# Optimization experiments

Hardware: AMD Instinct MI355X
Metric: run time of the kernel (lower is better)

The kernel has to match this reference:

```python
import jax, jax.numpy as jnp
import numpy as np
from jax import lax


def _ramp_filter_real(size):
    # torch ramp_filter: spatial-domain ramp, FFT is purely real (even symmetric)
    image_n = np.concatenate([np.arange(1, size // 2 + 1, 2),
                              np.arange(size // 2 - 1, 0, -2)]).astype(np.float64)
    f = np.zeros(size, dtype=np.float64)
    f[0] = 0.25
    f[1::2] = -1.0 / (np.pi * image_n) ** 2
    return (2.0 * np.real(np.fft.fft(f))).astype(np.float32)  # [size]


def setup_inputs() -> dict:
    key = jax.random.key(0)
    # sinogram: [B, C, detector_bins, n_angles]
    x = jax.random.normal(key, (4, 1, 512, 180), dtype=jnp.float32)
    return {"x": x}


def reference(x):
    B, C, S, A = x.shape  # S = in_size = it_size (circle=True), A = n_angles
    # ---- ramp filtering along detector axis (axis=2) ----
    pad_to = max(64, 1 << int(np.ceil(np.log2(2 * S))))
    xp = jnp.pad(x, ((0, 0), (0, 0), (0, pad_to - S), (0, 0)))
    ramp = jnp.asarray(_ramp_filter_real(pad_to))
    # original multiplies by complex filter r*(1+i); imag part of ifft is 0 for real x,
    # so real part equals standard ramp filtering
    Xf = jnp.fft.fft(xp, axis=2)
    filt = (ramp * (1.0 + 1.0j)).astype(jnp.complex64)
    xfilt = jnp.real(jnp.fft.ifft(Xf * filt[None, None, :, None], axis=2))
    xfilt = xfilt[:, :, :S, :].astype(x.dtype)  # [B,C,S,A]

    # ---- backprojection ----
    unit = jnp.linspace(-1.0, 1.0, S, dtype=x.dtype)
    ygrid, xgrid = jnp.meshgrid(unit, unit, indexing="ij")  # torch.meshgrid 'ij'
    thetas = (jnp.arange(A, dtype=x.dtype) * (np.pi / 180.0)).astype(x.dtype)
    # t coordinate in [-sqrt2, sqrt2]: [A,S,S]
    t = (xgrid[None] * jnp.cos(thetas)[:, None, None]
         - ygrid[None] * jnp.sin(thetas)[:, None, None])
    # grid_sample bilinear, align_corners=True, zeros padding; X coord selects angle i exactly
    p = (t + 1.0) * 0.5 * (S - 1)
    p0 = jnp.floor(p)
    w = (p - p0).astype(x.dtype)
    i0 = p0.astype(jnp.int32)
    i1 = i0 + 1
    v0 = ((i0 >= 0) & (i0 < S)).astype(x.dtype)
    v1 = ((i1 >= 0) & (i1 < S)).astype(x.dtype)
    i0c = jnp.clip(i0, 0, S - 1)
    i1c = jnp.clip(i1, 0, S - 1)

    xa = jnp.moveaxis(xfilt, 3, 0)  # [A,B,C,S]

    def body(acc, inp):
        xa_a, i0a, i1a, wa, v0a, v1a = inp
        g = (xa_a[:, :, i0a] * v0a * (1.0 - wa)
             + xa_a[:, :, i1a] * v1a * wa)  # [B,C,S,S]
        return acc + g, None

    reco0 = jnp.zeros((B, C, S, S), dtype=x.dtype)
    reco, _ = lax.scan(body, reco0, (xa, i0c, i1c, w, v0, v1))

    # circle mask + normalization
    mask = (xgrid ** 2 + ygrid ** 2) <= 1.0
    reco = jnp.where(mask[None, None], reco, 0.0)
    reco = reco * (np.pi / (2.0 * A))
    return reco
```

## Files before the change

kernel.cpp:

```cpp
#include <hip/hip_runtime.h>
#include <hip/hip_fp16.h>
#include <math.h>

namespace {

constexpr int BB  = 4;
constexpr int SS  = 512;
constexpr int AA  = 180;
constexpr int NJ  = 91;
constexpr int RST = 520;

__global__ __launch_bounds__(256) void ramp_zero_kernel(
    const float* __restrict__ x, uint2* __restrict__ xf, float* __restrict__ out) {
  const int t = threadIdx.x;
  const int k = blockIdx.x;
  const int b = blockIdx.y;
  {
    const int bid = b * NJ + k;
    float4 z = make_float4(0.f, 0.f, 0.f, 0.f);
    for (int i = bid * 256 + t; i < (BB * SS * SS) / 4; i += 364 * 256)
      ((float4*)out)[i] = z;
  }
  const int a1 = (k < 89) ? (k + 1) : ((k == 89) ? 0 : 90);
  const int a2 = (k < 89) ? (179 - k) : a1;

  __shared__ __align__(16) float xs[2][2][256];
  __shared__ __align__(16) float G[2][528];
  __shared__ float yb[2][512];

  const float s  = (float)(M_PI / 360.0);
  const float cc = (float)(-2.0 / (M_PI * M_PI)) * s;
  for (int i = t; i < 528; i += 256) {
    { int kk = i;     float d = (float)(2 * kk - 511); G[0][i] = (kk < 512) ? cc / (d * d) : 0.0f; }
    { int kk = i + 1; float d = (float)(2 * kk - 511); G[1][i] = (kk < 512) ? cc / (d * d) : 0.0f; }
  }

  const float* xb = x + (size_t)b * (SS * AA);
  {
    int m = t;
    xs[0][m & 1][m >> 1] = xb[(size_t)m * AA + a1];
    xs[1][m & 1][m >> 1] = xb[(size_t)m * AA + a2];
    m = t + 256;
    xs[0][m & 1][m >> 1] = xb[(size_t)m * AA + a1];
    xs[1][m & 1][m >> 1] = xb[(size_t)m * AA + a2];
  }
  __syncthreads();

  const int col = t >> 7;
  const int p   = (t >> 6) & 1;
  const int idx = t & 63;
  const float* Gp = G[p];
  const float* xv = xs[col][1 - p];

  float acc[4] = {0.f, 0.f, 0.f, 0.f};
  float W[8];
  {
    const int A0 = 4 * idx + 252;
    float4 w0 = *(const float4*)(Gp + A0);
    float4 w1 = *(const float4*)(Gp + A0 + 4);
    W[0] = w0.x; W[1] = w0.y; W[2] = w0.z; W[3] = w0.w;
    W[4] = w1.x; W[5] = w1.y; W[6] = w1.z; W[7] = w1.w;
  }

#pragma unroll
  for (int q = 0; q < 64; ++q) {
    const float4 xq = *(const float4*)(xv + 4 * q);
    float4 nw;
    if (q != 63) nw = *(const float4*)(Gp + (4 * idx + 252 - 4 * (q + 1)));
#pragma unroll
    for (int r = 0; r < 4; ++r) {
      acc[r] = fmaf(W[3 + r], xq.x, acc[r]);
      acc[r] = fmaf(W[2 + r], xq.y, acc[r]);
      acc[r] = fmaf(W[1 + r], xq.z, acc[r]);
      acc[r] = fmaf(W[0 + r], xq.w, acc[r]);
    }
    if (q != 63) {
      W[7] = W[3]; W[6] = W[2]; W[5] = W[1]; W[4] = W[0];
      W[0] = nw.x; W[1] = nw.y; W[2] = nw.z; W[3] = nw.w;
    }
  }

  const float selfc = 0.5f * s;
  const float* xsp = xs[col][p];
#pragma unroll
  for (int r = 0; r < 4; ++r)
    yb[col][p + 8 * idx + 2 * r] = fmaf(selfc, xsp[4 * idx + r], acc[r]);
  __syncthreads();

  uint2* orow = xf + (size_t)(b * NJ + k) * RST;
  const bool dual = (k < 89);
#pragma unroll
  for (int e = 0; e < 2; ++e) {
    int j = t + e * 256;
    __half2 lo = __floats2half2_rn(yb[0][j], yb[0][511 - j]);
    __half2 hi = dual ? __floats2half2_rn(yb[1][j], yb[1][511 - j])
                      : __floats2half2_rn(0.f, 0.f);
    uint2 u;
    __builtin_memcpy(&u.x, &lo, 4);
    __builtin_memcpy(&u.y, &hi, 4);
    orow[4 + j] = u;
  }
  if (t < 8) orow[(t < 4) ? t : (512 + t)] = make_uint2(0u, 0u);
}

__global__ __launch_bounds__(256, 4) void backproject_kernel(
    const uint2* __restrict__ xf, float* __restrict__ out) {
  __shared__ __align__(16) uint2 bufs[4][2][RST];
  __shared__ float2 trigS[23];

  const int t    = threadIdx.x;
  const int w    = t >> 6;
  const int lane = t & 63;
  const int tx   = blockIdx.x;
  const int ty   = blockIdx.y;
  const int b    = blockIdx.z >> 2;
  const int c    = blockIdx.z & 3;
  const int njobs = (c < 3) ? 23 : 22;

  const float step = 2.0f / 511.0f;
  {
    float x1 = -1.0f + (float)(tx * 64 + 63) * step;
    float y1 = -1.0f + (float)(ty * 16 + 15) * step;
    if (x1 * x1 + y1 * y1 > 1.0f) return;
  }

  if (t < njobs) {
    int k = c + 4 * t;
    int a = (k < 89) ? (k + 1) : ((k == 89) ? 0 : 90);
    float sn, cn;
    sincosf((float)a * (float)(M_PI / 180.0), &sn, &cn);
    trigS[t] = make_float2(cn * 255.5f, sn * 255.5f);
  }
  __syncthreads();

  const uint2* rows = xf + (size_t)b * NJ * RST;
  auto dma = [&](int i, int nb) {
    const char* g0 = (const char*)(rows + (size_t)(c + 4 * i) * RST);
    char* l0 = (char*)&bufs[w][nb][0];
#pragma unroll
    for (int sg = 0; sg < 4; ++sg)
      __builtin_amdgcn_global_load_lds(
          (const __attribute__((address_space(1))) void*)(g0 + sg * 1024 + lane * 16),
          (__attribute__((address_space(3))) void*)(l0 + sg * 1024), 16, 0, 0);
    if (lane < 4)
      __builtin_amdgcn_global_load_lds(
          (const __attribute__((address_space(1))) void*)(g0 + 4096 + lane * 16),
          (__attribute__((address_space(3))) void*)(l0 + 4096), 16, 0, 0);
  };

  const int gx = tx * 64 + lane;
  const float xg = __fadd_rn(-1.0f, __fmul_rn((float)gx, step));
  float yg[4];
#pragma unroll
  for (int kk = 0; kk < 4; ++kk)
    yg[kk] = __fadd_rn(-1.0f, __fmul_rn((float)(ty * 16 + w * 4 + kk), step));

  const float Kb = 255.5f + 4.0f;
  const __half2 hz = __floats2half2_rn(0.f, 0.f);
  float f00[4] = {0, 0, 0, 0}, f11[4] = {0, 0, 0, 0};
  float f01[4] = {0, 0, 0, 0}, f10[4] = {0, 0, 0, 0};
  __half2 accA[4], accB[4], accC[4], accD[4];
#pragma unroll
  for (int kk = 0; kk < 4; ++kk) { accA[kk] = hz; accB[kk] = hz; accC[kk] = hz; accD[kk] = hz; }

  dma(0, 0);

  for (int i = 0; i < njobs; ++i) {
    const bool more = (i + 1 < njobs);
    if (more) {
      dma(i + 1, (i + 1) & 1);
      __builtin_amdgcn_s_waitcnt(0x0F75);
    } else {
      __builtin_amdgcn_s_waitcnt(0x0F70);
    }

    const float2 cs = trigS[i];
    const float m = fmaf(xg, cs.x, Kb);
    const uint2* R = bufs[w][i & 1];
#pragma unroll
    for (int kk = 0; kk < 4; ++kk) {
      float P1 = fmaf(-yg[kk], cs.y, m);
      float Pu = fmaf( yg[kk], cs.y, m);
      int I1 = (int)P1, Iu = (int)Pu;
#if __has_builtin(__builtin_amdgcn_fractf)
      float w1 = __builtin_amdgcn_fractf(P1);
      float wu = __builtin_amdgcn_fractf(Pu);
#else
      float w1 = P1 - floorf(P1);
      float wu = Pu - floorf(Pu);
#endif
      auto w1r = __builtin_amdgcn_cvt_pkrtz(w1, w1);
      auto wur = __builtin_amdgcn_cvt_pkrtz(wu, wu);
      __half2 w1h, wuh;
      __builtin_memcpy(&w1h, &w1r, 4);
      __builtin_memcpy(&wuh, &wur, 4);
      struct alignas(8) Q { __half2 lo, hi, lo2, hi2; } q1, qu;
      __builtin_memcpy(&q1, R + I1, 16);
      __builtin_memcpy(&qu, R + Iu, 16);
      accA[kk] = __hadd2(accA[kk], __hfma2(w1h, __hsub2(q1.lo2, q1.lo), q1.lo));
      accB[kk] = __hadd2(accB[kk], __hfma2(w1h, __hsub2(q1.hi2, q1.hi), q1.hi));
      accC[kk] = __hadd2(accC[kk], __hfma2(wuh, __hsub2(qu.lo2, qu.lo), qu.lo));
      accD[kk] = __hadd2(accD[kk], __hfma2(wuh, __hsub2(qu.hi2, qu.hi), qu.hi));
    }

    if ((i % 5) == 4 || i == njobs - 1) {
#pragma unroll
      for (int kk = 0; kk < 4; ++kk) {
        float2 fa = __half22float2(accA[kk]);
        float2 fb = __half22float2(accB[kk]);
        float2 fc = __half22float2(accC[kk]);
        float2 fd = __half22float2(accD[kk]);
        f00[kk] += fa.x + fd.y;
        f11[kk] += fa.y + fd.x;
        f10[kk] += fb.x + fc.y;
        f01[kk] += fb.y + fc.x;
        accA[kk] = hz; accB[kk] = hz; accC[kk] = hz; accD[kk] = hz;
      }
    }
  }

  const int gxm  = 511 - gx;
  const float xgm = __fadd_rn(-1.0f, __fmul_rn((float)gxm, step));
  const float xx  = __fmul_rn(xg, xg);
  const float xxm = __fmul_rn(xgm, xgm);
#pragma unroll
  for (int kk = 0; kk < 4; ++kk) {
    int gy = ty * 16 + w * 4 + kk, gym = 511 - gy;
    float ygv = yg[kk];
    float ygm = __fadd_rn(-1.0f, __fmul_rn((float)gym, step));
    float yy  = __fmul_rn(ygv, ygv), yym = __fmul_rn(ygm, ygm);
    if (__fadd_rn(xx,  yy)  <= 1.0f) unsafeAtomicAdd(&out[((size_t)b * SS + gy ) * SS + gx ], f00[kk]);
    if (__fadd_rn(xxm, yym) <= 1.0f) unsafeAtomicAdd(&out[((size_t)b * SS + gym) * SS + gxm], f11[kk]);
    if (__fadd_rn(xx,  yym) <= 1.0f) unsafeAtomicAdd(&out[((size_t)b * SS + gym) * SS + gx ], f01[kk]);
    if (__fadd_rn(xxm, yy)  <= 1.0f) unsafeAtomicAdd(&out[((size_t)b * SS + gy ) * SS + gxm], f10[kk]);
  }
}

}

extern "C" void kernel_launch(void* const* d_in, const int* in_sizes, int n_in,
                              void* d_out, int out_size, void* d_ws, size_t ws_size,
                              hipStream_t stream) {
  const float* x   = (const float*)d_in[0];
  float*       out = (float*)d_out;
  uint2*       xf  = (uint2*)d_ws;

  ramp_zero_kernel<<<dim3(NJ, BB), 256, 0, stream>>>(x, xf, out);
  backproject_kernel<<<dim3(4, 16, 16), 256, 0, stream>>>(xf, out);
}
```

Measured before the change: 91.62 us.

## Pack neighbor samples into 16-byte rows and share one LDS buffer per block

The ramp kernel now writes each detector bin as a uint4 holding both the sample and its next neighbour for two angle pairs. This drops the padded 520-entry rows and the front offset. The backprojection kernel uses one block-wide double buffer instead of a private buffer per wave, splitting each row load across the four waves. Blocks cover 8 image rows instead of 16, so the grid doubles and the kernel targets higher occupancy. Syncing switches from per-wave waitcnt to __syncthreads, and without the padding, edge pixels outside the circle can read slightly past a row's end.

New measurement: 91.21 us. Within noise of the previous version (-0.4%).

```diff
diff --git a/kernel.cpp b/kernel.cpp
--- a/kernel.cpp
+++ b/kernel.cpp
@@ -8,10 +8,9 @@
 constexpr int SS  = 512;
 constexpr int AA  = 180;
 constexpr int NJ  = 91;
-constexpr int RST = 520;
 
 __global__ __launch_bounds__(256) void ramp_zero_kernel(
-    const float* __restrict__ x, uint2* __restrict__ xf, float* __restrict__ out) {
+    const float* __restrict__ x, uint4* __restrict__ xf, float* __restrict__ out) {
   const int t = threadIdx.x;
   const int k = blockIdx.x;
   const int b = blockIdx.y;
@@ -87,25 +86,38 @@
     yb[col][p + 8 * idx + 2 * r] = fmaf(selfc, xsp[4 * idx + r], acc[r]);
   __syncthreads();
 
-  uint2* orow = xf + (size_t)(b * NJ + k) * RST;
+  uint4* orow = xf + (size_t)(b * NJ + k) * 512;
   const bool dual = (k < 89);
 #pragma unroll
   for (int e = 0; e < 2; ++e) {
     int j = t + e * 256;
-    __half2 lo = __floats2half2_rn(yb[0][j], yb[0][511 - j]);
-    __half2 hi = dual ? __floats2half2_rn(yb[1][j], yb[1][511 - j])
-                      : __floats2half2_rn(0.f, 0.f);
-    uint2 u;
-    __builtin_memcpy(&u.x, &lo, 4);
-    __builtin_memcpy(&u.y, &hi, 4);
-    orow[4 + j] = u;
-  }
-  if (t < 8) orow[(t < 4) ? t : (512 + t)] = make_uint2(0u, 0u);
-}
-
-__global__ __launch_bounds__(256, 4) void backproject_kernel(
-    const uint2* __restrict__ xf, float* __restrict__ out) {
-  __shared__ __align__(16) uint2 bufs[4][2][RST];
+    float Aj  = yb[0][j];
+    float Ar  = yb[0][511 - j];
+    float Aj1 = (j < 511) ? yb[0][j + 1]   : 0.f;
+    float Ar1 = (j < 511) ? yb[0][510 - j] : 0.f;
+    float Bj = 0.f, Br = 0.f, Bj1 = 0.f, Br1 = 0.f;
+    if (dual) {
+      Bj  = yb[1][j];
+      Br  = yb[1][511 - j];
+      Bj1 = (j < 511) ? yb[1][j + 1]   : 0.f;
+      Br1 = (j < 511) ? yb[1][510 - j] : 0.f;
+    }
+    __half2 lo0 = __floats2half2_rn(Aj,  Ar);
+    __half2 lo1 = __floats2half2_rn(Bj,  Br);
+    __half2 hi0 = __floats2half2_rn(Aj1, Ar1);
+    __half2 hi1 = __floats2half2_rn(Bj1, Br1);
+    uint4 u;
+    __builtin_memcpy(&u.x, &lo0, 4);
+    __builtin_memcpy(&u.y, &lo1, 4);
+    __builtin_memcpy(&u.z, &hi0, 4);
+    __builtin_memcpy(&u.w, &hi1, 4);
+    orow[j] = u;
+  }
+}
+
+__global__ __launch_bounds__(256, 8) void backproject_kernel(
+    const uint4* __restrict__ xf, float* __restrict__ out) {
+  __shared__ __align__(16) uint4 bufs[2][512];
   __shared__ float2 trigS[23];
 
   const int t    = threadIdx.x;
@@ -115,12 +127,12 @@
   const int ty   = blockIdx.y;
   const int b    = blockIdx.z >> 2;
   const int c    = blockIdx.z & 3;
-  const int njobs = (c < 3) ? 23 : 22;
+  const int njobs = (91 - c + 3) >> 2;
 
   const float step = 2.0f / 511.0f;
   {
     float x1 = -1.0f + (float)(tx * 64 + 63) * step;
-    float y1 = -1.0f + (float)(ty * 16 + 15) * step;
+    float y1 = -1.0f + (float)(ty * 8 + 7) * step;
     if (x1 * x1 + y1 * y1 > 1.0f) return;
   }
 
@@ -131,54 +143,46 @@
     sincosf((float)a * (float)(M_PI / 180.0), &sn, &cn);
     trigS[t] = make_float2(cn * 255.5f, sn * 255.5f);
   }
-  __syncthreads();
-
-  const uint2* rows = xf + (size_t)b * NJ * RST;
+
+  const uint4* rows = xf + (size_t)b * NJ * 512;
   auto dma = [&](int i, int nb) {
-    const char* g0 = (const char*)(rows + (size_t)(c + 4 * i) * RST);
-    char* l0 = (char*)&bufs[w][nb][0];
-#pragma unroll
-    for (int sg = 0; sg < 4; ++sg)
-      __builtin_amdgcn_global_load_lds(
-          (const __attribute__((address_space(1))) void*)(g0 + sg * 1024 + lane * 16),
-          (__attribute__((address_space(3))) void*)(l0 + sg * 1024), 16, 0, 0);
-    if (lane < 4)
-      __builtin_amdgcn_global_load_lds(
-          (const __attribute__((address_space(1))) void*)(g0 + 4096 + lane * 16),
-          (__attribute__((address_space(3))) void*)(l0 + 4096), 16, 0, 0);
+    const char* g0 = (const char*)(rows + (size_t)(c + 4 * i) * 512);
+    char* l0 = (char*)&bufs[nb][0];
+    __builtin_amdgcn_global_load_lds(
+        (const __attribute__((address_space(1))) void*)(g0 + w * 1024 + lane * 16),
+        (__attribute__((address_space(3))) void*)(l0 + w * 1024), 16, 0, 0);
+    __builtin_amdgcn_global_load_lds(
+        (const __attribute__((address_space(1))) void*)(g0 + (w + 4) * 1024 + lane * 16),
+        (__attribute__((address_space(3))) void*)(l0 + (w + 4) * 1024), 16, 0, 0);
   };
 
   const int gx = tx * 64 + lane;
   const float xg = __fadd_rn(-1.0f, __fmul_rn((float)gx, step));
-  float yg[4];
-#pragma unroll
-  for (int kk = 0; kk < 4; ++kk)
-    yg[kk] = __fadd_rn(-1.0f, __fmul_rn((float)(ty * 16 + w * 4 + kk), step));
-
-  const float Kb = 255.5f + 4.0f;
+  float yg[2];
+#pragma unroll
+  for (int kk = 0; kk < 2; ++kk)
+    yg[kk] = __fadd_rn(-1.0f, __fmul_rn((float)(ty * 8 + w * 2 + kk), step));
+
+  const float Kb = 255.5f;
   const __half2 hz = __floats2half2_rn(0.f, 0.f);
-  float f00[4] = {0, 0, 0, 0}, f11[4] = {0, 0, 0, 0};
-  float f01[4] = {0, 0, 0, 0}, f10[4] = {0, 0, 0, 0};
-  __half2 accA[4], accB[4], accC[4], accD[4];
-#pragma unroll
-  for (int kk = 0; kk < 4; ++kk) { accA[kk] = hz; accB[kk] = hz; accC[kk] = hz; accD[kk] = hz; }
+  float f00[2] = {0, 0}, f11[2] = {0, 0}, f01[2] = {0, 0}, f10[2] = {0, 0};
+  __half2 accA[2], accB[2], accC[2], accD[2];
+#pragma unroll
+  for (int kk = 0; kk < 2; ++kk) { accA[kk] = hz; accB[kk] = hz; accC[kk] = hz; accD[kk] = hz; }
 
   dma(0, 0);
-
+  __syncthreads();
+
+  int buf = 0;
   for (int i = 0; i < njobs; ++i) {
     const bool more = (i + 1 < njobs);
-    if (more) {
-      dma(i + 1, (i + 1) & 1);
-      __builtin_amdgcn_s_waitcnt(0x0F75);
-    } else {
-      __builtin_amdgcn_s_waitcnt(0x0F70);
-    }
+    if (more) dma(i + 1, buf ^ 1);
 
     const float2 cs = trigS[i];
     const float m = fmaf(xg, cs.x, Kb);
-    const uint2* R = bufs[w][i & 1];
-#pragma unroll
-    for (int kk = 0; kk < 4; ++kk) {
+    const uint4* R = bufs[buf];
+#pragma unroll
+    for (int kk = 0; kk < 2; ++kk) {
       float P1 = fmaf(-yg[kk], cs.y, m);
       float Pu = fmaf( yg[kk], cs.y, m);
       int I1 = (int)P1, Iu = (int)Pu;
@@ -194,7 +198,7 @@
       __half2 w1h, wuh;
       __builtin_memcpy(&w1h, &w1r, 4);
       __builtin_memcpy(&wuh, &wur, 4);
-      struct alignas(8) Q { __half2 lo, hi, lo2, hi2; } q1, qu;
+      struct alignas(16) Q { __half2 lo, hi, lo2, hi2; } q1, qu;
       __builtin_memcpy(&q1, R + I1, 16);
       __builtin_memcpy(&qu, R + Iu, 16);
       accA[kk] = __hadd2(accA[kk], __hfma2(w1h, __hsub2(q1.lo2, q1.lo), q1.lo));
@@ -205,7 +209,7 @@
 
     if ((i % 5) == 4 || i == njobs - 1) {
 #pragma unroll
-      for (int kk = 0; kk < 4; ++kk) {
+      for (int kk = 0; kk < 2; ++kk) {
         float2 fa = __half22float2(accA[kk]);
         float2 fb = __half22float2(accB[kk]);
         float2 fc = __half22float2(accC[kk]);
@@ -217,6 +221,11 @@
         accA[kk] = hz; accB[kk] = hz; accC[kk] = hz; accD[kk] = hz;
       }
     }
+
+    if (more) {
+      __syncthreads();
+      buf ^= 1;
+    }
   }
 
   const int gxm  = 511 - gx;
@@ -224,8 +233,8 @@
   const float xx  = __fmul_rn(xg, xg);
   const float xxm = __fmul_rn(xgm, xgm);
 #pragma unroll
-  for (int kk = 0; kk < 4; ++kk) {
-    int gy = ty * 16 + w * 4 + kk, gym = 511 - gy;
+  for (int kk = 0; kk < 2; ++kk) {
+    int gy = ty * 8 + w * 2 + kk, gym = 511 - gy;
     float ygv = yg[kk];
     float ygm = __fadd_rn(-1.0f, __fmul_rn((float)gym, step));
     float yy  = __fmul_rn(ygv, ygv), yym = __fmul_rn(ygm, ygm);
@@ -243,8 +252,8 @@
                               hipStream_t stream) {
   const float* x   = (const float*)d_in[0];
   float*       out = (float*)d_out;
-  uint2*       xf  = (uint2*)d_ws;
+  uint4*       xf  = (uint4*)d_ws;
 
   ramp_zero_kernel<<<dim3(NJ, BB), 256, 0, stream>>>(x, xf, out);
-  backproject_kernel<<<dim3(4, 16, 16), 256, 0, stream>>>(xf, out);
-}
+  backproject_kernel<<<dim3(4, 32, 16), 256, 0, stream>>>(xf, out);
+}
```
